# Performance work log

Hardware: AMD Instinct MI355X
Metric: run time of the kernel (lower is better)

## Reference

```python
import jax, jax.numpy as jnp
import numpy as np

SEQ, BATCH, HIDDEN = 2048, 2, 2048
NUM_HEADS = 16
HEAD_DIM = HIDDEN // NUM_HEADS  # 128


def setup_inputs() -> dict:
    key = jax.random.key(0)
    k1, k2, k3, k4, k5 = jax.random.split(key, 5)
    scale = 1.0 / np.sqrt(HIDDEN)
    return {
        "hidden_states": jax.random.normal(k1, (SEQ, BATCH, HIDDEN), dtype=jnp.float32),
        "w_qkv": jax.random.normal(k2, (3 * HIDDEN, HIDDEN), dtype=jnp.float32) * scale,
        "b_qkv": jax.random.normal(k3, (3 * HIDDEN,), dtype=jnp.float32) * 0.01,
        "w_dense": jax.random.normal(k4, (HIDDEN, HIDDEN), dtype=jnp.float32) * scale,
        "b_dense": jax.random.normal(k5, (HIDDEN,), dtype=jnp.float32) * 0.01,
    }


def reference(hidden_states, w_qkv, b_qkv, w_dense, b_dense):
    s, b, H = hidden_states.shape
    nh, d = NUM_HEADS, HEAD_DIM
    norm_factor = jnp.asarray(np.sqrt(d), dtype=hidden_states.dtype)

    # QKV projection: [s, b, 3H] -> [s, b, nh, 3d] -> chunk into q, k, v
    mixed = hidden_states @ w_qkv.T + b_qkv
    mixed = mixed.reshape(s, b, nh, 3 * d)
    q, k, v = jnp.split(mixed, 3, axis=-1)  # each [s, b, nh, d]

    # Causal scaled dot-product attention, materializing [b, nh, sq, sk]
    scores = jnp.einsum("sbhd,tbhd->bhst", q, k) / norm_factor
    causal = jnp.tril(jnp.ones((s, s), dtype=bool))  # [sq, sk]
    scores = jnp.where(causal[None, None, :, :], scores, jnp.asarray(-10000.0, scores.dtype))
    probs = jax.nn.softmax(scores, axis=-1)

    # Context: [s, b, nh, d] -> [s, b, H]
    ctx = jnp.einsum("bhst,tbhd->sbhd", probs, v).reshape(s, b, H)

    # Output projection
    return ctx @ w_dense.T + b_dense
```

## Files before the change

### kernel.cpp

```cpp
#include <hip/hip_runtime.h>
#include <stdint.h>
#include <stddef.h>

#define SEQ   2048
#define BATCH 2
#define HID   2048
#define NH    16
#define HD    128
#define MTOT  (SEQ*BATCH)
#define NQKV  (3*HID)
#define KDIM  HID
#define LOG2E 1.4426950408889634f

#define BK64    64
#define NT64    (KDIM/BK64)

typedef short  bf16x8 __attribute__((ext_vector_type(8)));
typedef float  f32x4  __attribute__((ext_vector_type(4)));

__device__ __forceinline__ unsigned short f2bf(float f) {
  union { float f; uint32_t u; } a; a.f = f;
  uint32_t r = a.u + 0x7fffu + ((a.u >> 16) & 1u);
  return (unsigned short)(r >> 16);
}

__device__ __forceinline__ f32x4 mfma16(bf16x8 a, bf16x8 b, f32x4 c) {
  return __builtin_amdgcn_mfma_f32_16x16x32_bf16(a, b, c, 0, 0, 0);
}

__device__ __forceinline__ void gl_lds16(const unsigned short* g, unsigned short* l) {
  __builtin_amdgcn_global_load_lds(
      (const __attribute__((address_space(1))) void*)g,
      (__attribute__((address_space(3))) void*)l, 16, 0, 0);
}

__global__ void cvt3_f32_bf16(const float* __restrict__ a, unsigned short* __restrict__ oa, int na,
                              const float* __restrict__ b, unsigned short* __restrict__ ob, int nb,
                              const float* __restrict__ c, unsigned short* __restrict__ oc, int nc) {
  int i = blockIdx.x * blockDim.x + threadIdx.x;
  int stride = gridDim.x * blockDim.x;
  int ntot = na + nb + nc;
  for (; i < ntot; i += stride) {
    const float* src; unsigned short* dst; int j;
    if (i < na)           { src = a; dst = oa; j = i; }
    else if (i < na + nb) { src = b; dst = ob; j = i - na; }
    else                  { src = c; dst = oc; j = i - na - nb; }
    float4 f = reinterpret_cast<const float4*>(src)[j];
    ushort4 o;
    o.x = f2bf(f.x); o.y = f2bf(f.y); o.z = f2bf(f.z); o.w = f2bf(f.w);
    reinterpret_cast<ushort4*>(dst)[j] = o;
  }
}

__global__ __launch_bounds__(256) void transpose_v(
    const unsigned short* __restrict__ V, unsigned short* __restrict__ Vt) {
  __shared__ unsigned short tile[64][72];
  const int t  = threadIdx.x;
  const int bh = blockIdx.z;
  const int s0 = blockIdx.x * 64;
  const int d0 = blockIdx.y * 64;
  const size_t vb = (size_t)bh * SEQ * HD;
  const size_t tb = (size_t)bh * HD * SEQ;
#pragma unroll
  for (int p = 0; p < 2; ++p) {
    int r = p * 32 + (t >> 3);
    *(uint4*)&tile[r][(t & 7) * 8] =
        *(const uint4*)&V[vb + (size_t)(s0 + r) * HD + d0 + (t & 7) * 8];
  }
  __syncthreads();
#pragma unroll
  for (int p = 0; p < 2; ++p) {
    int dr = p * 32 + (t >> 3);
    int sc = (t & 7) * 8;
    unsigned short tmp[8];
#pragma unroll
    for (int e = 0; e < 8; ++e) tmp[e] = tile[sc + e][dr];
    *(uint4*)&Vt[tb + (size_t)(d0 + dr) * SEQ + s0 + sc] = *(const uint4*)tmp;
  }
}


#define QBUFS 28672

#define G8_SB()  asm volatile("s_barrier" ::: "memory")
#define G8_LGKM() do { asm volatile("s_waitcnt lgkmcnt(0)" ::: "memory");     \
                       __builtin_amdgcn_sched_barrier(0); } while (0)

#define G8_RDA(G) do {                                                        \
    p0 = *(const bf16x8*)&sb[abase + (2*(G)    ) * 1024 + ga0];               \
    p1 = *(const bf16x8*)&sb[abase + (2*(G)    ) * 1024 + ga1];               \
    p2 = *(const bf16x8*)&sb[abase + (2*(G) + 1) * 1024 + ga0];               \
    p3 = *(const bf16x8*)&sb[abase + (2*(G) + 1) * 1024 + ga1];               \
  } while (0)

#define G8_MFMA(G) do {                                                       \
    __builtin_amdgcn_s_setprio(1);                                            \
    _Pragma("unroll")                                                         \
    for (int n_ = 0; n_ < 3; ++n_) {                                          \
      acc[2*(G)][n_]     = mfma16(p0, bq0[n_], acc[2*(G)][n_]);               \
      acc[2*(G)][n_]     = mfma16(p1, bq1[n_], acc[2*(G)][n_]);               \
      acc[2*(G) + 1][n_] = mfma16(p2, bq0[n_], acc[2*(G) + 1][n_]);           \
      acc[2*(G) + 1][n_] = mfma16(p3, bq1[n_], acc[2*(G) + 1][n_]);           \
    }                                                                         \
    __builtin_amdgcn_sched_barrier(0);                                        \
    __builtin_amdgcn_s_setprio(0);                                            \
  } while (0)

#define G8_STA(R) gl_lds16(Asrc + (size_t)(R) * KDIM + koff,                  \
                           &db[((R) + w * 8) * 64])
#define G8_STB(R) gl_lds16(Bsrc + (size_t)(R) * KDIM + koff,                  \
                           &db[16384 + ((R) + w * 8) * 64])

#define G8_TILE(DOSTAGE, VM1, VM3) do {                                       \
    bf16x8 bq0[3], bq1[3], p0, p1, p2, p3;                                    \
                                                       \
    _Pragma("unroll")                                                         \
    for (int n_ = 0; n_ < 3; ++n_) {                                          \
      bq0[n_] = *(const bf16x8*)&sb[bbase + n_ * 1024 + ga0];                 \
      bq1[n_] = *(const bf16x8*)&sb[bbase + n_ * 1024 + ga1];                 \
    }                                                                         \
    G8_RDA(0);                                                                \
    if (DOSTAGE) { G8_STB(0); G8_STB(64); }                                   \
    G8_SB(); G8_LGKM();                                                       \
    G8_MFMA(0);                                                               \
    G8_SB();                                                                  \
                                                       \
    G8_RDA(1);                                                                \
    if (DOSTAGE) { G8_STB(128); G8_STA(0); }                                  \
    asm volatile("s_waitcnt " VM1 ::: "memory");                              \
    G8_SB(); G8_LGKM();                                                       \
    G8_MFMA(1);                                                               \
    G8_SB();                                                                  \
                                                       \
    G8_RDA(2);                                                                \
    if (DOSTAGE) { G8_STA(128); G8_STA(64); }                                 \
    G8_SB(); G8_LGKM();                                                       \
    G8_MFMA(2);                                                               \
    G8_SB();                                                                  \
                                                       \
    G8_RDA(3);                                                                \
    if (DOSTAGE) { G8_STA(192); }                                             \
    asm volatile("s_waitcnt " VM3 ::: "memory");                              \
    G8_SB(); G8_LGKM();                                                       \
    G8_MFMA(3);                                                               \
    G8_SB();                                                                  \
  } while (0)

__global__ __launch_bounds__(512, 2) void qkv_gemm(
    const unsigned short* __restrict__ A,
    const unsigned short* __restrict__ B,
    const float* __restrict__ bias,
    unsigned short* __restrict__ Qo,
    unsigned short* __restrict__ Ko,
    unsigned short* __restrict__ Vo)
{
  __shared__ unsigned short smb[2 * QBUFS];
  const int id  = blockIdx.x;
  const int swz = (id & 7) * 64 + (id >> 3);
  const int m0 = (swz >> 5) * 256, n0 = (swz & 31) * 192;
  const int t = threadIdx.x, l = t & 63, w = t >> 6;
  const int wm = w >> 2, wn = w & 3;
  const int fr = l & 15, fg = l >> 4;
  const int abase = (wm * 128 + fr) * 64;
  const int bbase = 16384 + (wn * 48 + fr) * 64;
  const int ga0 = ((fg     ) ^ (fr & 7)) * 8;
  const int ga1 = ((fg + 4 ) ^ (fr & 7)) * 8;
  const int srcrow = w * 8 + (l >> 3);
  const int sgr    = ((l & 7) ^ (l >> 3)) * 8;
  const unsigned short* Asrc = A + (size_t)(m0 + srcrow) * KDIM + sgr;
  const unsigned short* Bsrc = B + (size_t)(n0 + srcrow) * KDIM + sgr;
  f32x4 acc[8][3] = {};

  {
    unsigned short* db = smb;
    size_t koff = 0;
    G8_STB(0); G8_STB(64); G8_STB(128);
    G8_STA(0); G8_STA(128); G8_STA(64); G8_STA(192);
  }
  asm volatile("s_waitcnt vmcnt(2)" ::: "memory");
  asm volatile("s_barrier" ::: "memory");

#pragma unroll 1
  for (int kt = 0; kt < NT64 - 1; ++kt) {
    const unsigned short* sb = &smb[(kt & 1) * QBUFS];
    unsigned short* db = &smb[((kt + 1) & 1) * QBUFS];
    size_t koff = (size_t)(kt + 1) * BK64;
    G8_TILE(1, "vmcnt(4)", "vmcnt(2)");
  }
  {
    const unsigned short* sb = &smb[((NT64 - 1) & 1) * QBUFS];
    unsigned short* db = smb;
    size_t koff = 0; (void)koff;
    G8_TILE(0, "vmcnt(0)", "vmcnt(0)");
  }

#pragma unroll
  for (int n = 0; n < 3; ++n) {
    int ncol = n0 + wn * 48 + n * 16 + fr;
    float bv = bias[ncol];
    int head = ncol / 384;
    int rem  = ncol - head * 384;
    int wi   = rem >> 7;
    int d    = rem & 127;
    unsigned short* dst = (wi == 0) ? Qo : ((wi == 1) ? Ko : Vo);
#pragma unroll
    for (int m = 0; m < 8; ++m) {
#pragma unroll
      for (int j = 0; j < 4; ++j) {
        int r = m0 + wm * 128 + m * 16 + fg * 4 + j;
        int s = r >> 1, bb = r & 1;
        float val = acc[m][n][j] + bv;
        if (wi == 0) val *= 0.08838834764831845f;
        dst[(((size_t)(bb * NH + head)) * SEQ + s) * HD + d] = f2bf(val);
      }
    }
  }
}


#define GEMM_PRE()                                                            \
  const int t = threadIdx.x, l = t & 63, w = t >> 6;                          \
  const int wm = w >> 1, wn = w & 1;                                          \
  const int fr = l & 15, fg = l >> 4;                                         \
  const int fx = fr & 7;                                                      \
  const int srow = l >> 3;                                                    \
  const int sgr  = ((l & 7) ^ srow) * 8;                                      \
  const unsigned short* Aw = A + (size_t)(m0 + w * 32 + srow) * KDIM + sgr;   \
  const unsigned short* Bw = B + (size_t)(n0 + w * 16 + srow) * KDIM + sgr;   \
  unsigned short* smb = &sm[0][0];                                            \
  const int a0 = (wm * 64 + fr) * 64 + ((fg ^ fx) * 8);                       \
  const int a1 = (wm * 64 + fr) * 64 + (((4 + fg) ^ fx) * 8);                 \
  const int b0 = 16384 + (wn * 64 + fr) * 64 + ((fg ^ fx) * 8);               \
  const int b1 = 16384 + (wn * 64 + fr) * 64 + (((4 + fg) ^ fx) * 8);         \
  f32x4 acc[4][4] = {};

#define STAGE_AB(KT) do {                                                     \
    unsigned short* dst = &smb[((KT) % 3) * 24576];                           \
    const unsigned short* ap = Aw + (size_t)(KT) * BK64;                      \
    gl_lds16(ap,                    &dst[(w * 4 + 0) * 512]);                 \
    gl_lds16(ap + 8  * KDIM,        &dst[(w * 4 + 1) * 512]);                 \
    gl_lds16(ap + 16 * KDIM,        &dst[(w * 4 + 2) * 512]);                 \
    gl_lds16(ap + 24 * KDIM,        &dst[(w * 4 + 3) * 512]);                 \
    const unsigned short* bp = Bw + (size_t)(KT) * BK64;                      \
    gl_lds16(bp,                    &dst[16384 + (w * 2 + 0) * 512]);         \
    gl_lds16(bp + 8 * KDIM,         &dst[16384 + (w * 2 + 1) * 512]);         \
  } while (0)

#define GEMM_BODY(KT, VM, DOSTAGE) do {                                       \
    const unsigned short* sb = &smb[((KT) % 3) * 24576];                      \
    if (DOSTAGE) STAGE_AB((KT) + 2);                                          \
    bf16x8 af0[4], af1[4], bg0[4], bg1[4];                                    \
    _Pragma("unroll")                                                         \
    for (int m_ = 0; m_ < 4; ++m_) {                                          \
      af0[m_] = *(const bf16x8*)&sb[a0 + m_ * 1024];                          \
      af1[m_] = *(const bf16x8*)&sb[a1 + m_ * 1024];                          \
    }                                                                         \
    _Pragma("unroll")                                                         \
    for (int n_ = 0; n_ < 4; ++n_) {                                          \
      bg0[n_] = *(const bf16x8*)&sb[b0 + n_ * 1024];                          \
      bg1[n_] = *(const bf16x8*)&sb[b1 + n_ * 1024];                          \
    }                                                                         \
    asm volatile("s_waitcnt vmcnt(" #VM ")" ::: "memory");                    \
    asm volatile("s_barrier" ::: "memory");                                   \
    asm volatile("s_waitcnt lgkmcnt(0)" ::: "memory");                        \
    __builtin_amdgcn_sched_barrier(0);                                        \
    __builtin_amdgcn_s_setprio(1);                                            \
    _Pragma("unroll")                                                         \
    for (int m_ = 0; m_ < 4; ++m_)                                            \
      _Pragma("unroll")                                                       \
      for (int n_ = 0; n_ < 4; ++n_)                                          \
        acc[m_][n_] = mfma16(af0[m_], bg0[n_], acc[m_][n_]);                  \
    _Pragma("unroll")                                                         \
    for (int m_ = 0; m_ < 4; ++m_)                                            \
      _Pragma("unroll")                                                       \
      for (int n_ = 0; n_ < 4; ++n_)                                          \
        acc[m_][n_] = mfma16(af1[m_], bg1[n_], acc[m_][n_]);                  \
    __builtin_amdgcn_sched_barrier(0);                                        \
    __builtin_amdgcn_s_setprio(0);                                            \
    asm volatile("s_barrier" ::: "memory");                                   \
  } while (0)

#define GEMM_MAIN()                                                           \
  STAGE_AB(0); STAGE_AB(1);                                                   \
  asm volatile("s_waitcnt vmcnt(6)" ::: "memory");                            \
  asm volatile("s_barrier" ::: "memory");                                     \
  _Pragma("unroll 1")                                                         \
  for (int kt = 0; kt < NT64 - 2; ++kt)                                       \
    GEMM_BODY(kt, 6, 1);                                                      \
  GEMM_BODY(NT64 - 2, 0, 0);                                                  \
  GEMM_BODY(NT64 - 1, 0, 0);

__global__ __launch_bounds__(512, 1) void dense_gemm(
    const unsigned short* __restrict__ A,
    const unsigned short* __restrict__ B,
    const float* __restrict__ bias,
    float* __restrict__ out)
{
  __shared__ unsigned short sm[3][24576];
  int id  = blockIdx.x;
  int swz = (id & 7) * (gridDim.x >> 3) + (id >> 3);
  const int m0 = (swz / 16) * 256, n0 = (swz % 16) * 128;
  GEMM_PRE();
  GEMM_MAIN();

  const int g4 = fg * 4;
#pragma unroll
  for (int n = 0; n < 4; ++n) {
    int ncol = n0 + wn * 64 + n * 16 + fr;
    float bv = bias[ncol];
#pragma unroll
    for (int m = 0; m < 4; ++m) {
#pragma unroll
      for (int j = 0; j < 4; ++j) {
        int r = m0 + wm * 64 + m * 16 + g4 + j;
        out[(size_t)r * HID + ncol] = acc[m][n][j] + bv;
      }
    }
  }
}

__global__ __launch_bounds__(256, 2) void attn_fwd(
    const unsigned short* __restrict__ Q,
    const unsigned short* __restrict__ K,
    const unsigned short* __restrict__ Vt,
    unsigned short* __restrict__ ctx)
{
  __shared__ unsigned short Ksh[2][64 * 128];
  __shared__ unsigned short Vsh[2][128 * 64];
  __shared__ unsigned short Psh[4][16 * 72];
  const int t = threadIdx.x, l = t & 63, w = t >> 6;
  int nwg = gridDim.x * gridDim.y;
  int id  = blockIdx.y * gridDim.x + blockIdx.x;
  int swz = (id & 7) * (nwg >> 3) + (id >> 3);
  const int pair = swz & 15;
  const int bh   = swz >> 4;
  const int qtA = pair, qtB = 31 - pair;
  const int fr = l & 15, fg = l >> 4;
  const size_t base  = (size_t)bh * SEQ * HD;
  const size_t vbase = (size_t)bh * HD * SEQ;

#define STAGE(BUF, KT) do {                                                   \
    const unsigned short* Kt_ = K + base + (size_t)((KT) * 64) * HD;          \
    _Pragma("unroll")                                                         \
    for (int i_ = 0; i_ < 4; ++i_) {                                          \
      int ch_  = w * 4 + i_;                                                  \
      int row_ = ch_ * 4 + (l >> 4);                                          \
      int c16_ = (l & 15) ^ (row_ & 7);                                       \
      gl_lds16(Kt_ + (size_t)row_ * HD + c16_ * 8, &Ksh[BUF][ch_ * 512]);     \
    }                                                                         \
    const unsigned short* Vg_ = Vt + vbase + (KT) * 64;                       \
    _Pragma("unroll")                                                         \
    for (int i_ = 0; i_ < 4; ++i_) {                                          \
      int ch_  = w * 4 + i_;                                                  \
      int row_ = ch_ * 8 + (l >> 3);                                          \
      int c16_ = (l & 7) ^ (row_ & 7);                                        \
      gl_lds16(Vg_ + (size_t)row_ * SEQ + c16_ * 8, &Vsh[BUF][ch_ * 512]);    \
    }                                                                         \
  } while (0)

#define COMPUTE_TILE(QF, OACC, MROW, LROW, QT) do {                           \
    f32x4 sacc[4] = {};                                                       \
    _Pragma("unroll")                                                         \
    for (int c_ = 0; c_ < 4; ++c_) {                                          \
      _Pragma("unroll")                                                       \
      for (int n_ = 0; n_ < 4; ++n_) {                                        \
        int krow = n_ * 16 + fr;                                              \
        int g_   = (c_ * 4 + fg) ^ (krow & 7);                                \
        bf16x8 kf = *(const bf16x8*)&Ksh[buf][krow * 128 + g_ * 8];           \
        sacc[n_] = mfma16(QF[c_], kf, sacc[n_]);                              \
      }                                                                       \
    }                                                                         \
    if (kt == (QT)) {                                                         \
      _Pragma("unroll")                                                       \
      for (int n_ = 0; n_ < 4; ++n_)                                          \
        _Pragma("unroll")                                                     \
        for (int j_ = 0; j_ < 4; ++j_)                                        \
          if (n_ * 16 + fr > w * 16 + fg * 4 + j_) sacc[n_][j_] = -1e30f;     \
    }                                                                         \
    float tm_[4];                                                             \
    _Pragma("unroll")                                                         \
    for (int j_ = 0; j_ < 4; ++j_) {                                          \
      float v0 = fmaxf(fmaxf(sacc[0][j_], sacc[1][j_]),                       \
                       fmaxf(sacc[2][j_], sacc[3][j_]));                      \
      v0 = fmaxf(v0, __shfl_xor(v0, 1));                                      \
      v0 = fmaxf(v0, __shfl_xor(v0, 2));                                      \
      v0 = fmaxf(v0, __shfl_xor(v0, 4));                                      \
      v0 = fmaxf(v0, __shfl_xor(v0, 8));                                      \
      tm_[j_] = v0;                                                           \
    }                                                                         \
    float sc_[4], ps_[4];                                                     \
    _Pragma("unroll")                                                         \
    for (int j_ = 0; j_ < 4; ++j_) {                                          \
      float mn_ = fmaxf(MROW[j_], tm_[j_]);                                   \
      sc_[j_] = exp2f((MROW[j_] - mn_) * LOG2E);                              \
      MROW[j_] = mn_;                                                         \
      ps_[j_] = 0.f;                                                          \
    }                                                                         \
    _Pragma("unroll")                                                         \
    for (int n_ = 0; n_ < 4; ++n_)                                            \
      _Pragma("unroll")                                                       \
      for (int j_ = 0; j_ < 4; ++j_) {                                        \
        float p_ = exp2f((sacc[n_][j_] - MROW[j_]) * LOG2E);                  \
        sacc[n_][j_] = p_;                                                    \
        ps_[j_] += p_;                                                        \
      }                                                                       \
    _Pragma("unroll")                                                         \
    for (int j_ = 0; j_ < 4; ++j_) {                                          \
      float s_ = ps_[j_];                                                     \
      s_ += __shfl_xor(s_, 1);                                                \
      s_ += __shfl_xor(s_, 2);                                                \
      s_ += __shfl_xor(s_, 4);                                                \
      s_ += __shfl_xor(s_, 8);                                                \
      LROW[j_] = LROW[j_] * sc_[j_] + s_;                                     \
    }                                                                         \
    _Pragma("unroll")                                                         \
    for (int n_ = 0; n_ < 8; ++n_)                                            \
      _Pragma("unroll")                                                       \
      for (int j_ = 0; j_ < 4; ++j_)                                          \
        OACC[n_][j_] *= sc_[j_];                                              \
    _Pragma("unroll")                                                         \
    for (int n_ = 0; n_ < 4; ++n_)                                            \
      _Pragma("unroll")                                                       \
      for (int j_ = 0; j_ < 4; ++j_)                                          \
        Psh[w][(fg * 4 + j_) * 72 + n_ * 16 + fr] = f2bf(sacc[n_][j_]);       \
    _Pragma("unroll")                                                         \
    for (int ks_ = 0; ks_ < 2; ++ks_) {                                       \
      bf16x8 pf = *(const bf16x8*)&Psh[w][fr * 72 + ks_ * 32 + fg * 8];       \
      _Pragma("unroll")                                                       \
      for (int n_ = 0; n_ < 8; ++n_) {                                        \
        int vrow = n_ * 16 + fr;                                              \
        int g_   = (ks_ * 4 + fg) ^ (vrow & 7);                               \
        bf16x8 vf = *(const bf16x8*)&Vsh[buf][vrow * 64 + g_ * 8];            \
        OACC[n_] = mfma16(pf, vf, OACC[n_]);                                  \
      }                                                                       \
    }                                                                         \
  } while (0)

  bf16x8 qfA[4], qfB[4];
  {
    const unsigned short* qpA = Q + base + (size_t)(qtA * 64 + w * 16 + fr) * HD + fg * 8;
    const unsigned short* qpB = Q + base + (size_t)(qtB * 64 + w * 16 + fr) * HD + fg * 8;
#pragma unroll
    for (int c = 0; c < 4; ++c) {
      qfA[c] = *(const bf16x8*)(qpA + c * 32);
      qfB[c] = *(const bf16x8*)(qpB + c * 32);
    }
  }
  f32x4 oaccA[8] = {}, oaccB[8] = {};
  float mA[4] = {-1e30f, -1e30f, -1e30f, -1e30f};
  float mB[4] = {-1e30f, -1e30f, -1e30f, -1e30f};
  float lA[4] = {0.f, 0.f, 0.f, 0.f};
  float lB[4] = {0.f, 0.f, 0.f, 0.f};

  STAGE(0, 0);
  __syncthreads();
  int buf = 0;
  for (int kt = 0; kt <= qtB; ++kt) {
    if (kt < qtB) STAGE(buf ^ 1, kt + 1);
    COMPUTE_TILE(qfB, oaccB, mB, lB, qtB);
    if (kt <= qtA) COMPUTE_TILE(qfA, oaccA, mA, lA, qtA);
    __syncthreads();
    buf ^= 1;
  }

  const int bb = bh >> 4, h = bh & 15;
#define WRITE_CTX(OACC, LROW, QT) do {                                        \
    _Pragma("unroll")                                                         \
    for (int n_ = 0; n_ < 8; ++n_)                                            \
      _Pragma("unroll")                                                       \
      for (int j_ = 0; j_ < 4; ++j_) {                                        \
        int qrow = (QT) * 64 + w * 16 + fg * 4 + j_;                          \
        float val = OACC[n_][j_] / LROW[j_];                                  \
        ctx[((size_t)(qrow * BATCH + bb)) * HID + h * HD + n_ * 16 + fr] =    \
            f2bf(val);                                                        \
      }                                                                       \
  } while (0)
  WRITE_CTX(oaccA, lA, qtA);
  WRITE_CTX(oaccB, lB, qtB);
#undef STAGE
#undef COMPUTE_TILE
#undef WRITE_CTX
}

extern "C" void kernel_launch(void* const* d_in, const int* in_sizes, int n_in,
                              void* d_out, int out_size, void* d_ws, size_t ws_size,
                              hipStream_t stream) {
  const float* hs      = (const float*)d_in[0];
  const float* w_qkv   = (const float*)d_in[1];
  const float* b_qkv   = (const float*)d_in[2];
  const float* w_dense = (const float*)d_in[3];
  const float* b_dense = (const float*)d_in[4];
  float* out = (float*)d_out;

  unsigned short* hsb = (unsigned short*)d_ws;
  unsigned short* wqb = hsb + (size_t)MTOT * HID;
  unsigned short* wdb = wqb + (size_t)NQKV * HID;
  unsigned short* q   = wdb + (size_t)HID * HID;
  unsigned short* k   = q   + (size_t)MTOT * HID;
  unsigned short* v   = k   + (size_t)MTOT * HID;
  unsigned short* ctx = v   + (size_t)MTOT * HID;
  unsigned short* vt  = hsb;

  cvt3_f32_bf16<<<2048, 256, 0, stream>>>(
      hs, hsb, (MTOT * HID) / 4,
      w_qkv, wqb, (NQKV * HID) / 4,
      w_dense, wdb, (HID * HID) / 4);

  qkv_gemm<<<dim3((MTOT / 256) * (NQKV / 192)), 512, 0, stream>>>(hsb, wqb, b_qkv, q, k, v);
  transpose_v<<<dim3(SEQ / 64, HD / 64, BATCH * NH), 256, 0, stream>>>(v, vt);
  attn_fwd<<<dim3(16, 32), 256, 0, stream>>>(q, k, vt, ctx);
  dense_gemm<<<dim3((MTOT / 256) * (HID / 128)), 512, 0, stream>>>(ctx, wdb, b_dense, out);
}
```

Measured before the change: 275.0 us.

## Fuse V transpose into QKV epilogue and software-pipeline LDS fragment reads

The separate transpose_v kernel is removed. The QKV GEMM epilogue now writes V directly in transposed [bh, d, s] layout, which saves a launch and a full read/write pass over V. The GEMM main loop is restructured to double-buffer register fragments: the next phase's A and B fragments are read from LDS while the current phase's MFMAs run, with the loop unrolled by two tiles. The transposed V stores are strided by SEQ and poorly coalesced, and the extra fragment registers may raise register pressure.

```diff
diff --git a/kernel.cpp b/kernel.cpp
--- a/kernel.cpp
+++ b/kernel.cpp
@@ -52,98 +52,56 @@
   }
 }
 
-__global__ __launch_bounds__(256) void transpose_v(
-    const unsigned short* __restrict__ V, unsigned short* __restrict__ Vt) {
-  __shared__ unsigned short tile[64][72];
-  const int t  = threadIdx.x;
-  const int bh = blockIdx.z;
-  const int s0 = blockIdx.x * 64;
-  const int d0 = blockIdx.y * 64;
-  const size_t vb = (size_t)bh * SEQ * HD;
-  const size_t tb = (size_t)bh * HD * SEQ;
-#pragma unroll
-  for (int p = 0; p < 2; ++p) {
-    int r = p * 32 + (t >> 3);
-    *(uint4*)&tile[r][(t & 7) * 8] =
-        *(const uint4*)&V[vb + (size_t)(s0 + r) * HD + d0 + (t & 7) * 8];
-  }
-  __syncthreads();
-#pragma unroll
-  for (int p = 0; p < 2; ++p) {
-    int dr = p * 32 + (t >> 3);
-    int sc = (t & 7) * 8;
-    unsigned short tmp[8];
-#pragma unroll
-    for (int e = 0; e < 8; ++e) tmp[e] = tile[sc + e][dr];
-    *(uint4*)&Vt[tb + (size_t)(d0 + dr) * SEQ + s0 + sc] = *(const uint4*)tmp;
-  }
-}
-
 
 #define QBUFS 28672
 
-#define G8_SB()  asm volatile("s_barrier" ::: "memory")
-#define G8_LGKM() do { asm volatile("s_waitcnt lgkmcnt(0)" ::: "memory");     \
-                       __builtin_amdgcn_sched_barrier(0); } while (0)
-
-#define G8_RDA(G) do {                                                        \
-    p0 = *(const bf16x8*)&sb[abase + (2*(G)    ) * 1024 + ga0];               \
-    p1 = *(const bf16x8*)&sb[abase + (2*(G)    ) * 1024 + ga1];               \
-    p2 = *(const bf16x8*)&sb[abase + (2*(G) + 1) * 1024 + ga0];               \
-    p3 = *(const bf16x8*)&sb[abase + (2*(G) + 1) * 1024 + ga1];               \
-  } while (0)
-
-#define G8_MFMA(G) do {                                                       \
+#define QSTA(R) gl_lds16(Asrc + (size_t)(R) * KDIM + koff, &db[((R) + w * 8) * 64])
+#define QSTB(R) gl_lds16(Bsrc + (size_t)(R) * KDIM + koff, &db[16384 + ((R) + w * 8) * 64])
+
+#define RD_A4(R0_,R1_,R2_,R3_, G, SB) do {                                    \
+    R0_ = *(const bf16x8*)&(SB)[abase + (2*(G)    ) * 1024 + ga0];            \
+    R1_ = *(const bf16x8*)&(SB)[abase + (2*(G)    ) * 1024 + ga1];            \
+    R2_ = *(const bf16x8*)&(SB)[abase + (2*(G) + 1) * 1024 + ga0];            \
+    R3_ = *(const bf16x8*)&(SB)[abase + (2*(G) + 1) * 1024 + ga1];            \
+  } while (0)
+
+#define RD_B6(BQ, SB) do {                                                    \
+    BQ[0] = *(const bf16x8*)&(SB)[bbase + 0 * 1024 + ga0];                    \
+    BQ[1] = *(const bf16x8*)&(SB)[bbase + 1 * 1024 + ga0];                    \
+    BQ[2] = *(const bf16x8*)&(SB)[bbase + 2 * 1024 + ga0];                    \
+    BQ[3] = *(const bf16x8*)&(SB)[bbase + 0 * 1024 + ga1];                    \
+    BQ[4] = *(const bf16x8*)&(SB)[bbase + 1 * 1024 + ga1];                    \
+    BQ[5] = *(const bf16x8*)&(SB)[bbase + 2 * 1024 + ga1];                    \
+  } while (0)
+
+#define QPH(G, A0_,A1_,A2_,A3_, RDOP, STOP, VMOP, BQ) do {                    \
+    STOP;                                                                     \
+    VMOP;                                                                     \
+    asm volatile("s_barrier" ::: "memory");                                   \
+    RDOP;                                                                     \
+    __builtin_amdgcn_sched_barrier(0);                                        \
     __builtin_amdgcn_s_setprio(1);                                            \
     _Pragma("unroll")                                                         \
     for (int n_ = 0; n_ < 3; ++n_) {                                          \
-      acc[2*(G)][n_]     = mfma16(p0, bq0[n_], acc[2*(G)][n_]);               \
-      acc[2*(G)][n_]     = mfma16(p1, bq1[n_], acc[2*(G)][n_]);               \
-      acc[2*(G) + 1][n_] = mfma16(p2, bq0[n_], acc[2*(G) + 1][n_]);           \
-      acc[2*(G) + 1][n_] = mfma16(p3, bq1[n_], acc[2*(G) + 1][n_]);           \
+      acc[2*(G)][n_]     = mfma16(A0_, BQ[n_],     acc[2*(G)][n_]);           \
+      acc[2*(G)][n_]     = mfma16(A1_, BQ[n_ + 3], acc[2*(G)][n_]);           \
+      acc[2*(G) + 1][n_] = mfma16(A2_, BQ[n_],     acc[2*(G) + 1][n_]);       \
+      acc[2*(G) + 1][n_] = mfma16(A3_, BQ[n_ + 3], acc[2*(G) + 1][n_]);       \
     }                                                                         \
     __builtin_amdgcn_sched_barrier(0);                                        \
     __builtin_amdgcn_s_setprio(0);                                            \
-  } while (0)
-
-#define G8_STA(R) gl_lds16(Asrc + (size_t)(R) * KDIM + koff,                  \
-                           &db[((R) + w * 8) * 64])
-#define G8_STB(R) gl_lds16(Bsrc + (size_t)(R) * KDIM + koff,                  \
-                           &db[16384 + ((R) + w * 8) * 64])
-
-#define G8_TILE(DOSTAGE, VM1, VM3) do {                                       \
-    bf16x8 bq0[3], bq1[3], p0, p1, p2, p3;                                    \
-                                                       \
-    _Pragma("unroll")                                                         \
-    for (int n_ = 0; n_ < 3; ++n_) {                                          \
-      bq0[n_] = *(const bf16x8*)&sb[bbase + n_ * 1024 + ga0];                 \
-      bq1[n_] = *(const bf16x8*)&sb[bbase + n_ * 1024 + ga1];                 \
-    }                                                                         \
-    G8_RDA(0);                                                                \
-    if (DOSTAGE) { G8_STB(0); G8_STB(64); }                                   \
-    G8_SB(); G8_LGKM();                                                       \
-    G8_MFMA(0);                                                               \
-    G8_SB();                                                                  \
-                                                       \
-    G8_RDA(1);                                                                \
-    if (DOSTAGE) { G8_STB(128); G8_STA(0); }                                  \
-    asm volatile("s_waitcnt " VM1 ::: "memory");                              \
-    G8_SB(); G8_LGKM();                                                       \
-    G8_MFMA(1);                                                               \
-    G8_SB();                                                                  \
-                                                       \
-    G8_RDA(2);                                                                \
-    if (DOSTAGE) { G8_STA(128); G8_STA(64); }                                 \
-    G8_SB(); G8_LGKM();                                                       \
-    G8_MFMA(2);                                                               \
-    G8_SB();                                                                  \
-                                                       \
-    G8_RDA(3);                                                                \
-    if (DOSTAGE) { G8_STA(192); }                                             \
-    asm volatile("s_waitcnt " VM3 ::: "memory");                              \
-    G8_SB(); G8_LGKM();                                                       \
-    G8_MFMA(3);                                                               \
-    G8_SB();                                                                  \
+    asm volatile("s_barrier" ::: "memory");                                   \
+  } while (0)
+
+#define VM4  asm volatile("s_waitcnt vmcnt(4)" ::: "memory")
+#define VM2  asm volatile("s_waitcnt vmcnt(2)" ::: "memory")
+#define VM0  asm volatile("s_waitcnt vmcnt(0)" ::: "memory")
+
+#define QTILE(SB, BQC, ST0, ST1, ST2, ST3, VP1, VP3, RAOP) do {               \
+    QPH(0, aX0,aX1,aX2,aX3, RD_A4(aY0,aY1,aY2,aY3, 1, SB), ST0, (void)0, BQC);\
+    QPH(1, aY0,aY1,aY2,aY3, RD_A4(aX0,aX1,aX2,aX3, 2, SB), ST1, VP1,     BQC);\
+    QPH(2, aX0,aX1,aX2,aX3, RD_A4(aY0,aY1,aY2,aY3, 3, SB), ST2, (void)0, BQC);\
+    QPH(3, aY0,aY1,aY2,aY3, RAOP,                          ST3, VP3,     BQC);\
   } while (0)
 
 __global__ __launch_bounds__(512, 2) void qkv_gemm(
@@ -152,7 +110,7 @@
     const float* __restrict__ bias,
     unsigned short* __restrict__ Qo,
     unsigned short* __restrict__ Ko,
-    unsigned short* __restrict__ Vo)
+    unsigned short* __restrict__ Vt)
 {
   __shared__ unsigned short smb[2 * QBUFS];
   const int id  = blockIdx.x;
@@ -169,29 +127,65 @@
   const int sgr    = ((l & 7) ^ (l >> 3)) * 8;
   const unsigned short* Asrc = A + (size_t)(m0 + srcrow) * KDIM + sgr;
   const unsigned short* Bsrc = B + (size_t)(n0 + srcrow) * KDIM + sgr;
+  unsigned short* const buf0 = smb;
+  unsigned short* const buf1 = smb + QBUFS;
+
   f32x4 acc[8][3] = {};
+  bf16x8 aX0, aX1, aX2, aX3, aY0, aY1, aY2, aY3;
+  bf16x8 bqE[6], bqO[6];
 
   {
-    unsigned short* db = smb;
+    unsigned short* db = buf0;
     size_t koff = 0;
-    G8_STB(0); G8_STB(64); G8_STB(128);
-    G8_STA(0); G8_STA(128); G8_STA(64); G8_STA(192);
-  }
-  asm volatile("s_waitcnt vmcnt(2)" ::: "memory");
+    QSTB(0); QSTB(64); QSTB(128);
+    QSTA(0); QSTA(128); QSTA(64); QSTA(192);
+  }
+  VM2;
   asm volatile("s_barrier" ::: "memory");
+  RD_B6(bqE, buf0);
+  RD_A4(aX0, aX1, aX2, aX3, 0, buf0);
 
 #pragma unroll 1
-  for (int kt = 0; kt < NT64 - 1; ++kt) {
-    const unsigned short* sb = &smb[(kt & 1) * QBUFS];
-    unsigned short* db = &smb[((kt + 1) & 1) * QBUFS];
-    size_t koff = (size_t)(kt + 1) * BK64;
-    G8_TILE(1, "vmcnt(4)", "vmcnt(2)");
+  for (int tp = 0; tp < 15; ++tp) {
+    {
+      unsigned short* db = buf1;
+      size_t koff = (size_t)(2 * tp + 1) * BK64;
+      QTILE(buf0, bqE,
+            QSTB(0); QSTB(64),
+            QSTB(128); QSTA(0),
+            QSTA(128); QSTA(64),
+            QSTA(192),
+            VM4, VM2,
+            RD_B6(bqO, buf1); RD_A4(aX0,aX1,aX2,aX3, 0, buf1));
+    }
+    {
+      unsigned short* db = buf0;
+      size_t koff = (size_t)(2 * tp + 2) * BK64;
+      QTILE(buf1, bqO,
+            QSTB(0); QSTB(64),
+            QSTB(128); QSTA(0),
+            QSTA(128); QSTA(64),
+            QSTA(192),
+            VM4, VM2,
+            RD_B6(bqE, buf0); RD_A4(aX0,aX1,aX2,aX3, 0, buf0));
+    }
   }
   {
-    const unsigned short* sb = &smb[((NT64 - 1) & 1) * QBUFS];
-    unsigned short* db = smb;
-    size_t koff = 0; (void)koff;
-    G8_TILE(0, "vmcnt(0)", "vmcnt(0)");
+    unsigned short* db = buf1;
+    size_t koff = (size_t)31 * BK64;
+    QTILE(buf0, bqE,
+          QSTB(0); QSTB(64),
+          QSTB(128); QSTA(0),
+          QSTA(128); QSTA(64),
+          QSTA(192),
+          VM4, VM2,
+          RD_B6(bqO, buf1); RD_A4(aX0,aX1,aX2,aX3, 0, buf1));
+  }
+  {
+    QTILE(buf1, bqO,
+          (void)0, (void)0, (void)0, (void)0,
+          VM0, (void)0,
+          (void)0);
   }
 
 #pragma unroll
@@ -202,7 +196,6 @@
     int rem  = ncol - head * 384;
     int wi   = rem >> 7;
     int d    = rem & 127;
-    unsigned short* dst = (wi == 0) ? Qo : ((wi == 1) ? Ko : Vo);
 #pragma unroll
     for (int m = 0; m < 8; ++m) {
 #pragma unroll
@@ -210,8 +203,14 @@
         int r = m0 + wm * 128 + m * 16 + fg * 4 + j;
         int s = r >> 1, bb = r & 1;
         float val = acc[m][n][j] + bv;
-        if (wi == 0) val *= 0.08838834764831845f;
-        dst[(((size_t)(bb * NH + head)) * SEQ + s) * HD + d] = f2bf(val);
+        if (wi == 0) {
+          val *= 0.08838834764831845f;
+          Qo[(((size_t)(bb * NH + head)) * SEQ + s) * HD + d] = f2bf(val);
+        } else if (wi == 1) {
+          Ko[(((size_t)(bb * NH + head)) * SEQ + s) * HD + d] = f2bf(val);
+        } else {
+          Vt[(((size_t)(bb * NH + head)) * HD + d) * SEQ + s] = f2bf(val);
+        }
       }
     }
   }
@@ -497,17 +496,15 @@
   unsigned short* wdb = wqb + (size_t)NQKV * HID;
   unsigned short* q   = wdb + (size_t)HID * HID;
   unsigned short* k   = q   + (size_t)MTOT * HID;
-  unsigned short* v   = k   + (size_t)MTOT * HID;
-  unsigned short* ctx = v   + (size_t)MTOT * HID;
-  unsigned short* vt  = hsb;
+  unsigned short* vt  = k   + (size_t)MTOT * HID;
+  unsigned short* ctx = vt  + (size_t)MTOT * HID;
 
   cvt3_f32_bf16<<<2048, 256, 0, stream>>>(
       hs, hsb, (MTOT * HID) / 4,
       w_qkv, wqb, (NQKV * HID) / 4,
       w_dense, wdb, (HID * HID) / 4);
 
-  qkv_gemm<<<dim3((MTOT / 256) * (NQKV / 192)), 512, 0, stream>>>(hsb, wqb, b_qkv, q, k, v);
-  transpose_v<<<dim3(SEQ / 64, HD / 64, BATCH * NH), 256, 0, stream>>>(v, vt);
+  qkv_gemm<<<dim3((MTOT / 256) * (NQKV / 192)), 512, 0, stream>>>(hsb, wqb, b_qkv, q, k, vt);
   attn_fwd<<<dim3(16, 32), 256, 0, stream>>>(q, k, vt, ctx);
   dense_gemm<<<dim3((MTOT / 256) * (HID / 128)), 512, 0, stream>>>(ctx, wdb, b_dense, out);
 }
```

New measurement: 279.9 us. No clear change (+1.8%).

## Restructure attention into one q-tile per block with 32-key tiles and direct V loads

Applied to the files above, without the earlier changes.

The attention kernel no longer pairs two q-tiles per block (qtA/qtB balancing). It now launches 1024 blocks, each handling one 64-row q-tile, scheduled longest-first. Each block walks 32-key tiles with K staged in LDS, while V fragments are loaded straight from global into registers instead of through LDS. LDS use shrinks and launch bounds rise to 3 blocks per SM to raise occupancy, at the cost of more loop iterations, more global V traffic and the loss of the paired load balancing. The GEMM staging macros are renamed only.

```diff
diff --git a/kernel.cpp b/kernel.cpp
--- a/kernel.cpp
+++ b/kernel.cpp
@@ -82,6 +82,9 @@
 
 #define QBUFS 28672
 
+#define QSTA(R) gl_lds16(Asrc + (size_t)(R) * KDIM + koff, &db[((R) + w * 8) * 64])
+#define QSTB(R) gl_lds16(Bsrc + (size_t)(R) * KDIM + koff, &db[16384 + ((R) + w * 8) * 64])
+
 #define G8_SB()  asm volatile("s_barrier" ::: "memory")
 #define G8_LGKM() do { asm volatile("s_waitcnt lgkmcnt(0)" ::: "memory");     \
                        __builtin_amdgcn_sched_barrier(0); } while (0)
@@ -106,11 +109,6 @@
     __builtin_amdgcn_s_setprio(0);                                            \
   } while (0)
 
-#define G8_STA(R) gl_lds16(Asrc + (size_t)(R) * KDIM + koff,                  \
-                           &db[((R) + w * 8) * 64])
-#define G8_STB(R) gl_lds16(Bsrc + (size_t)(R) * KDIM + koff,                  \
-                           &db[16384 + ((R) + w * 8) * 64])
-
 #define G8_TILE(DOSTAGE, VM1, VM3) do {                                       \
     bf16x8 bq0[3], bq1[3], p0, p1, p2, p3;                                    \
                                                        \
@@ -120,26 +118,26 @@
       bq1[n_] = *(const bf16x8*)&sb[bbase + n_ * 1024 + ga1];                 \
     }                                                                         \
     G8_RDA(0);                                                                \
-    if (DOSTAGE) { G8_STB(0); G8_STB(64); }                                   \
+    if (DOSTAGE) { QSTB(0); QSTB(64); }                                       \
     G8_SB(); G8_LGKM();                                                       \
     G8_MFMA(0);                                                               \
     G8_SB();                                                                  \
                                                        \
     G8_RDA(1);                                                                \
-    if (DOSTAGE) { G8_STB(128); G8_STA(0); }                                  \
+    if (DOSTAGE) { QSTB(128); QSTA(0); }                                      \
     asm volatile("s_waitcnt " VM1 ::: "memory");                              \
     G8_SB(); G8_LGKM();                                                       \
     G8_MFMA(1);                                                               \
     G8_SB();                                                                  \
                                                        \
     G8_RDA(2);                                                                \
-    if (DOSTAGE) { G8_STA(128); G8_STA(64); }                                 \
+    if (DOSTAGE) { QSTA(128); QSTA(64); }                                     \
     G8_SB(); G8_LGKM();                                                       \
     G8_MFMA(2);                                                               \
     G8_SB();                                                                  \
                                                        \
     G8_RDA(3);                                                                \
-    if (DOSTAGE) { G8_STA(192); }                                             \
+    if (DOSTAGE) { QSTA(192); }                                               \
     asm volatile("s_waitcnt " VM3 ::: "memory");                              \
     G8_SB(); G8_LGKM();                                                       \
     G8_MFMA(3);                                                               \
@@ -174,8 +172,8 @@
   {
     unsigned short* db = smb;
     size_t koff = 0;
-    G8_STB(0); G8_STB(64); G8_STB(128);
-    G8_STA(0); G8_STA(128); G8_STA(64); G8_STA(192);
+    QSTB(0); QSTB(64); QSTB(128);
+    QSTA(0); QSTA(128); QSTA(64); QSTA(192);
   }
   asm volatile("s_waitcnt vmcnt(2)" ::: "memory");
   asm volatile("s_barrier" ::: "memory");
@@ -319,167 +317,145 @@
   }
 }
 
-__global__ __launch_bounds__(256, 2) void attn_fwd(
+
+__global__ __launch_bounds__(256, 3) void attn_fwd(
     const unsigned short* __restrict__ Q,
     const unsigned short* __restrict__ K,
     const unsigned short* __restrict__ Vt,
     unsigned short* __restrict__ ctx)
 {
-  __shared__ unsigned short Ksh[2][64 * 128];
-  __shared__ unsigned short Vsh[2][128 * 64];
-  __shared__ unsigned short Psh[4][16 * 72];
+  __shared__ unsigned short Ksh[2][32 * 128];
+  __shared__ unsigned short Psh[4][16 * 40];
   const int t = threadIdx.x, l = t & 63, w = t >> 6;
-  int nwg = gridDim.x * gridDim.y;
-  int id  = blockIdx.y * gridDim.x + blockIdx.x;
-  int swz = (id & 7) * (nwg >> 3) + (id >> 3);
-  const int pair = swz & 15;
-  const int bh   = swz >> 4;
-  const int qtA = pair, qtB = 31 - pair;
+  const int id = blockIdx.x;
+  const int bh = (id & 7) * 4 + ((id >> 3) & 3);
+  const int qt = 31 - (id >> 5);
   const int fr = l & 15, fg = l >> 4;
   const size_t base  = (size_t)bh * SEQ * HD;
   const size_t vbase = (size_t)bh * HD * SEQ;
-
-#define STAGE(BUF, KT) do {                                                   \
-    const unsigned short* Kt_ = K + base + (size_t)((KT) * 64) * HD;          \
-    _Pragma("unroll")                                                         \
-    for (int i_ = 0; i_ < 4; ++i_) {                                          \
-      int ch_  = w * 4 + i_;                                                  \
+  const int NT = 2 * (qt + 1);
+
+#define STAGE32(BUF, KTT) do {                                                \
+    const unsigned short* Kt_ = K + base + (size_t)((KTT) * 32) * HD;         \
+    _Pragma("unroll")                                                         \
+    for (int i_ = 0; i_ < 2; ++i_) {                                          \
+      int ch_  = w * 2 + i_;                                                  \
       int row_ = ch_ * 4 + (l >> 4);                                          \
       int c16_ = (l & 15) ^ (row_ & 7);                                       \
       gl_lds16(Kt_ + (size_t)row_ * HD + c16_ * 8, &Ksh[BUF][ch_ * 512]);     \
     }                                                                         \
-    const unsigned short* Vg_ = Vt + vbase + (KT) * 64;                       \
-    _Pragma("unroll")                                                         \
-    for (int i_ = 0; i_ < 4; ++i_) {                                          \
-      int ch_  = w * 4 + i_;                                                  \
-      int row_ = ch_ * 8 + (l >> 3);                                          \
-      int c16_ = (l & 7) ^ (row_ & 7);                                        \
-      gl_lds16(Vg_ + (size_t)row_ * SEQ + c16_ * 8, &Vsh[BUF][ch_ * 512]);    \
-    }                                                                         \
-  } while (0)
-
-#define COMPUTE_TILE(QF, OACC, MROW, LROW, QT) do {                           \
-    f32x4 sacc[4] = {};                                                       \
-    _Pragma("unroll")                                                         \
-    for (int c_ = 0; c_ < 4; ++c_) {                                          \
-      _Pragma("unroll")                                                       \
-      for (int n_ = 0; n_ < 4; ++n_) {                                        \
-        int krow = n_ * 16 + fr;                                              \
-        int g_   = (c_ * 4 + fg) ^ (krow & 7);                                \
-        bf16x8 kf = *(const bf16x8*)&Ksh[buf][krow * 128 + g_ * 8];           \
-        sacc[n_] = mfma16(QF[c_], kf, sacc[n_]);                              \
-      }                                                                       \
-    }                                                                         \
-    if (kt == (QT)) {                                                         \
-      _Pragma("unroll")                                                       \
-      for (int n_ = 0; n_ < 4; ++n_)                                          \
-        _Pragma("unroll")                                                     \
-        for (int j_ = 0; j_ < 4; ++j_)                                        \
-          if (n_ * 16 + fr > w * 16 + fg * 4 + j_) sacc[n_][j_] = -1e30f;     \
-    }                                                                         \
-    float tm_[4];                                                             \
-    _Pragma("unroll")                                                         \
-    for (int j_ = 0; j_ < 4; ++j_) {                                          \
-      float v0 = fmaxf(fmaxf(sacc[0][j_], sacc[1][j_]),                       \
-                       fmaxf(sacc[2][j_], sacc[3][j_]));                      \
-      v0 = fmaxf(v0, __shfl_xor(v0, 1));                                      \
-      v0 = fmaxf(v0, __shfl_xor(v0, 2));                                      \
-      v0 = fmaxf(v0, __shfl_xor(v0, 4));                                      \
-      v0 = fmaxf(v0, __shfl_xor(v0, 8));                                      \
-      tm_[j_] = v0;                                                           \
-    }                                                                         \
-    float sc_[4], ps_[4];                                                     \
-    _Pragma("unroll")                                                         \
-    for (int j_ = 0; j_ < 4; ++j_) {                                          \
-      float mn_ = fmaxf(MROW[j_], tm_[j_]);                                   \
-      sc_[j_] = exp2f((MROW[j_] - mn_) * LOG2E);                              \
-      MROW[j_] = mn_;                                                         \
-      ps_[j_] = 0.f;                                                          \
-    }                                                                         \
-    _Pragma("unroll")                                                         \
-    for (int n_ = 0; n_ < 4; ++n_)                                            \
-      _Pragma("unroll")                                                       \
-      for (int j_ = 0; j_ < 4; ++j_) {                                        \
-        float p_ = exp2f((sacc[n_][j_] - MROW[j_]) * LOG2E);                  \
-        sacc[n_][j_] = p_;                                                    \
-        ps_[j_] += p_;                                                        \
-      }                                                                       \
-    _Pragma("unroll")                                                         \
-    for (int j_ = 0; j_ < 4; ++j_) {                                          \
-      float s_ = ps_[j_];                                                     \
-      s_ += __shfl_xor(s_, 1);                                                \
-      s_ += __shfl_xor(s_, 2);                                                \
-      s_ += __shfl_xor(s_, 4);                                                \
-      s_ += __shfl_xor(s_, 8);                                                \
-      LROW[j_] = LROW[j_] * sc_[j_] + s_;                                     \
-    }                                                                         \
-    _Pragma("unroll")                                                         \
-    for (int n_ = 0; n_ < 8; ++n_)                                            \
-      _Pragma("unroll")                                                       \
-      for (int j_ = 0; j_ < 4; ++j_)                                          \
-        OACC[n_][j_] *= sc_[j_];                                              \
-    _Pragma("unroll")                                                         \
-    for (int n_ = 0; n_ < 4; ++n_)                                            \
-      _Pragma("unroll")                                                       \
-      for (int j_ = 0; j_ < 4; ++j_)                                          \
-        Psh[w][(fg * 4 + j_) * 72 + n_ * 16 + fr] = f2bf(sacc[n_][j_]);       \
-    _Pragma("unroll")                                                         \
-    for (int ks_ = 0; ks_ < 2; ++ks_) {                                       \
-      bf16x8 pf = *(const bf16x8*)&Psh[w][fr * 72 + ks_ * 32 + fg * 8];       \
-      _Pragma("unroll")                                                       \
-      for (int n_ = 0; n_ < 8; ++n_) {                                        \
-        int vrow = n_ * 16 + fr;                                              \
-        int g_   = (ks_ * 4 + fg) ^ (vrow & 7);                               \
-        bf16x8 vf = *(const bf16x8*)&Vsh[buf][vrow * 64 + g_ * 8];            \
-        OACC[n_] = mfma16(pf, vf, OACC[n_]);                                  \
-      }                                                                       \
-    }                                                                         \
-  } while (0)
-
-  bf16x8 qfA[4], qfB[4];
+  } while (0)
+
+  bf16x8 qf[4];
   {
-    const unsigned short* qpA = Q + base + (size_t)(qtA * 64 + w * 16 + fr) * HD + fg * 8;
-    const unsigned short* qpB = Q + base + (size_t)(qtB * 64 + w * 16 + fr) * HD + fg * 8;
-#pragma unroll
-    for (int c = 0; c < 4; ++c) {
-      qfA[c] = *(const bf16x8*)(qpA + c * 32);
-      qfB[c] = *(const bf16x8*)(qpB + c * 32);
-    }
-  }
-  f32x4 oaccA[8] = {}, oaccB[8] = {};
-  float mA[4] = {-1e30f, -1e30f, -1e30f, -1e30f};
-  float mB[4] = {-1e30f, -1e30f, -1e30f, -1e30f};
-  float lA[4] = {0.f, 0.f, 0.f, 0.f};
-  float lB[4] = {0.f, 0.f, 0.f, 0.f};
-
-  STAGE(0, 0);
+    const unsigned short* qp =
+        Q + base + (size_t)(qt * 64 + w * 16 + fr) * HD + fg * 8;
+#pragma unroll
+    for (int c = 0; c < 4; ++c) qf[c] = *(const bf16x8*)(qp + c * 32);
+  }
+  f32x4 oacc[8] = {};
+  float mrow[4] = {-1e30f, -1e30f, -1e30f, -1e30f};
+  float lrow[4] = {0.f, 0.f, 0.f, 0.f};
+
+  STAGE32(0, 0);
   __syncthreads();
   int buf = 0;
-  for (int kt = 0; kt <= qtB; ++kt) {
-    if (kt < qtB) STAGE(buf ^ 1, kt + 1);
-    COMPUTE_TILE(qfB, oaccB, mB, lB, qtB);
-    if (kt <= qtA) COMPUTE_TILE(qfA, oaccA, mA, lA, qtA);
+
+#pragma unroll 1
+  for (int ktt = 0; ktt < NT; ++ktt) {
+    bf16x8 vf[8];
+    {
+      const unsigned short* vp = Vt + vbase + (size_t)fr * SEQ + ktt * 32 + fg * 8;
+#pragma unroll
+      for (int n2 = 0; n2 < 8; ++n2)
+        vf[n2] = *(const bf16x8*)(vp + (size_t)(n2 * 16) * SEQ);
+    }
+    if (ktt < NT - 1) STAGE32(buf ^ 1, ktt + 1);
+
+    f32x4 sacc[2] = {};
+#pragma unroll
+    for (int c = 0; c < 4; ++c) {
+#pragma unroll
+      for (int n = 0; n < 2; ++n) {
+        int krow = n * 16 + fr;
+        int g_   = (c * 4 + fg) ^ (krow & 7);
+        bf16x8 kf = *(const bf16x8*)&Ksh[buf][krow * 128 + g_ * 8];
+        sacc[n] = mfma16(qf[c], kf, sacc[n]);
+      }
+    }
+    if (ktt >= 2 * qt) {
+#pragma unroll
+      for (int n = 0; n < 2; ++n)
+#pragma unroll
+        for (int j = 0; j < 4; ++j) {
+          int key  = ktt * 32 + n * 16 + fr;
+          int qrow = qt * 64 + w * 16 + fg * 4 + j;
+          if (key > qrow) sacc[n][j] = -1e30f;
+        }
+    }
+    float tm[4];
+#pragma unroll
+    for (int j = 0; j < 4; ++j) {
+      float v0 = fmaxf(sacc[0][j], sacc[1][j]);
+      v0 = fmaxf(v0, __shfl_xor(v0, 1));
+      v0 = fmaxf(v0, __shfl_xor(v0, 2));
+      v0 = fmaxf(v0, __shfl_xor(v0, 4));
+      v0 = fmaxf(v0, __shfl_xor(v0, 8));
+      tm[j] = v0;
+    }
+    float scj[4], psum[4];
+#pragma unroll
+    for (int j = 0; j < 4; ++j) {
+      float mnew = fmaxf(mrow[j], tm[j]);
+      scj[j] = exp2f((mrow[j] - mnew) * LOG2E);
+      mrow[j] = mnew;
+      psum[j] = 0.f;
+    }
+#pragma unroll
+    for (int n = 0; n < 2; ++n)
+#pragma unroll
+      for (int j = 0; j < 4; ++j) {
+        float p = exp2f((sacc[n][j] - mrow[j]) * LOG2E);
+        sacc[n][j] = p;
+        psum[j] += p;
+      }
+#pragma unroll
+    for (int j = 0; j < 4; ++j) {
+      float s = psum[j];
+      s += __shfl_xor(s, 1);
+      s += __shfl_xor(s, 2);
+      s += __shfl_xor(s, 4);
+      s += __shfl_xor(s, 8);
+      lrow[j] = lrow[j] * scj[j] + s;
+    }
+#pragma unroll
+    for (int n2 = 0; n2 < 8; ++n2)
+#pragma unroll
+      for (int j = 0; j < 4; ++j)
+        oacc[n2][j] *= scj[j];
+#pragma unroll
+    for (int n = 0; n < 2; ++n)
+#pragma unroll
+      for (int j = 0; j < 4; ++j)
+        Psh[w][(fg * 4 + j) * 40 + n * 16 + fr] = f2bf(sacc[n][j]);
+    bf16x8 pf = *(const bf16x8*)&Psh[w][fr * 40 + fg * 8];
+#pragma unroll
+    for (int n2 = 0; n2 < 8; ++n2)
+      oacc[n2] = mfma16(pf, vf[n2], oacc[n2]);
     __syncthreads();
     buf ^= 1;
   }
 
   const int bb = bh >> 4, h = bh & 15;
-#define WRITE_CTX(OACC, LROW, QT) do {                                        \
-    _Pragma("unroll")                                                         \
-    for (int n_ = 0; n_ < 8; ++n_)                                            \
-      _Pragma("unroll")                                                       \
-      for (int j_ = 0; j_ < 4; ++j_) {                                        \
-        int qrow = (QT) * 64 + w * 16 + fg * 4 + j_;                          \
-        float val = OACC[n_][j_] / LROW[j_];                                  \
-        ctx[((size_t)(qrow * BATCH + bb)) * HID + h * HD + n_ * 16 + fr] =    \
-            f2bf(val);                                                        \
-      }                                                                       \
-  } while (0)
-  WRITE_CTX(oaccA, lA, qtA);
-  WRITE_CTX(oaccB, lB, qtB);
-#undef STAGE
-#undef COMPUTE_TILE
-#undef WRITE_CTX
+#pragma unroll
+  for (int n2 = 0; n2 < 8; ++n2)
+#pragma unroll
+    for (int j = 0; j < 4; ++j) {
+      int qrow = qt * 64 + w * 16 + fg * 4 + j;
+      float val = oacc[n2][j] / lrow[j];
+      ctx[((size_t)(qrow * BATCH + bb)) * HID + h * HD + n2 * 16 + fr] = f2bf(val);
+    }
+#undef STAGE32
 }
 
 extern "C" void kernel_launch(void* const* d_in, const int* in_sizes, int n_in,
@@ -508,6 +484,6 @@
 
   qkv_gemm<<<dim3((MTOT / 256) * (NQKV / 192)), 512, 0, stream>>>(hsb, wqb, b_qkv, q, k, v);
   transpose_v<<<dim3(SEQ / 64, HD / 64, BATCH * NH), 256, 0, stream>>>(v, vt);
-  attn_fwd<<<dim3(16, 32), 256, 0, stream>>>(q, k, vt, ctx);
+  attn_fwd<<<1024, 256, 0, stream>>>(q, k, vt, ctx);
   dense_gemm<<<dim3((MTOT / 256) * (HID / 128)), 512, 0, stream>>>(ctx, wdb, b_dense, out);
 }
```

Measured after the change: 331.7 us. 20.6% more time.
